# Performance work log

Hardware: AMD Instinct MI355X
Metric: run time of the kernel (lower is better)

The kernel has to match this reference:

```python
import jax, jax.numpy as jnp
import numpy as np

N = 100000   # nodes
E = 1600000  # edges (avg degree 16)
D = 128      # input_dim = embedding_dim = output_dim
NEG_SLOPE = 0.01  # nn.LeakyReLU default


def setup_inputs() -> dict:
    key = jax.random.key(0)
    k0, k1, k2, k3, k4, k5 = jax.random.split(key, 6)
    x = jax.random.normal(k0, (N, D), jnp.float32)
    edge_index = jax.random.randint(k1, (2, E), 0, N, dtype=jnp.int32)
    batch = jnp.zeros((N,), jnp.int32)
    # GCNConv params (glorot-ish scale)
    W1 = jax.random.normal(k2, (D, D), jnp.float32) * 0.05
    b1 = jax.random.normal(k3, (D,), jnp.float32) * 0.05
    W2 = jax.random.normal(k4, (D, D), jnp.float32) * 0.05
    b2 = jax.random.normal(k5, (D,), jnp.float32) * 0.05
    return {"x": x, "W1": W1, "b1": b1, "W2": W2, "b2": b2,
            "edge_index": edge_index, "batch": batch}


def _gcn_conv(x, W, b, src, dst, deg_isqrt):
    # x' = D^{-1/2} (A + I) D^{-1/2} (x W) + b   (PyG GCNConv defaults)
    h = x @ W                                   # [N, D]
    coef = deg_isqrt[src] * deg_isqrt[dst]      # [E]
    msg = h[src] * coef[:, None]                # [E, D] gather + scale
    out = jax.ops.segment_sum(msg, dst, num_segments=N)  # scatter-add
    out = out + h * (deg_isqrt * deg_isqrt)[:, None]      # self-loop term
    return out + b


def reference(x, W1, b1, W2, b2, edge_index, batch):
    src, dst = edge_index[0], edge_index[1]
    # degree on A + I (self loops), same for both layers
    deg = jax.ops.segment_sum(jnp.ones((E,), x.dtype), dst, num_segments=N) + 1.0
    deg_isqrt = jax.lax.rsqrt(deg)
    h = _gcn_conv(x, W1, b1, src, dst, deg_isqrt)
    h = jax.nn.leaky_relu(h, NEG_SLOPE)
    h = _gcn_conv(h, W2, b2, src, dst, deg_isqrt)
    return jax.nn.leaky_relu(h, NEG_SLOPE)
```

## Files before the change

kernel.cpp:

```cpp
#include <hip/hip_runtime.h>
#include <hip/hip_bf16.h>
#include <stdint.h>

#define NN 100000
#define NE 1600000
#define NR (NE + NN)
#define DD 128
#define NEG 0.01f
#define NB 391
#define CAPSH 13
#define NBLKE 391
#define NWB 65
#define GPAD 16

typedef __attribute__((ext_vector_type(8))) short short8;
typedef __attribute__((ext_vector_type(4))) float floatx4;
typedef __attribute__((ext_vector_type(4))) uint32_t uint32x4;

__device__ __forceinline__ uint16_t f2bf(float f){
  uint32_t i = __float_as_uint(f);
  return (uint16_t)((i + 0x7FFFu + ((i >> 16) & 1u)) >> 16);
}
__device__ __forceinline__ float lrelu(float x){ return fmaxf(x, NEG * x); }

__global__ __launch_bounds__(512) void k_init(const uint32_t* __restrict__ xw,
                                              int* __restrict__ flag,
                                              int* __restrict__ gcur){
  int t = threadIdx.x;
  for (int i = t; i < NB * GPAD; i += 512) gcur[i] = 0;
  if (t < 64){
    uint32_t w = xw[t];
    uint32_t e = (w >> 7) & 0xFFu;
    int plaus = (e >= 100u && e <= 134u) ? 1 : 0;
    unsigned long long b = __ballot(plaus);
    if (t == 0) flag[0] = (__popcll(b) >= 48) ? 0 : 1;
  }
}

__global__ __launch_bounds__(512) void k_scat1(const int* __restrict__ src,
                                               const int* __restrict__ dst,
                                               int* __restrict__ gcur,
                                               uint32_t* __restrict__ pairs,
                                               const void* __restrict__ W1,
                                               const void* __restrict__ W2,
                                               const void* __restrict__ b1,
                                               const void* __restrict__ b2,
                                               uint16_t* __restrict__ WT1,
                                               uint16_t* __restrict__ WT2,
                                               uint16_t* __restrict__ bb,
                                               const int* __restrict__ flag){
  int t = threadIdx.x, b = blockIdx.x;
  if (b >= NBLKE){
    int j = (b - NBLKE) * 512 + t;
    int f = flag[0];
    if (j < 16384){
      int c = j >> 7, k = j & 127;
      WT1[j] = f ? f2bf(((const float*)W1)[k * DD + c])
                 : ((const uint16_t*)W1)[k * DD + c];
    } else if (j < 32768){
      int q = j - 16384;
      int c = q >> 7, k = q & 127;
      WT2[q] = f ? f2bf(((const float*)W2)[k * DD + c])
                 : ((const uint16_t*)W2)[k * DD + c];
    } else if (j < 33024){
      int q = j - 32768;
      const void* sp = (q < 128) ? b1 : b2;
      int i2 = q & 127;
      bb[q] = f ? f2bf(((const float*)sp)[i2]) : ((const uint16_t*)sp)[i2];
    }
    return;
  }
  __shared__ int lh[NB];
  if (t < NB) lh[t] = 0;
  __syncthreads();
  int ds[8], ss[8];
  #pragma unroll
  for (int i = 0; i < 8; i++){
    int e = b * 4096 + i * 512 + t;
    if (e < NE){
      ds[i] = dst[e]; ss[i] = src[e];
      atomicAdd(&lh[ds[i] >> 8], 1);
    } else ds[i] = -1;
  }
  __syncthreads();
  if (t < NB){
    int c = lh[t];
    int base = c ? atomicAdd(&gcur[t * GPAD], c) : 0;
    lh[t] = (t << CAPSH) + base;
  }
  __syncthreads();
  #pragma unroll
  for (int i = 0; i < 8; i++){
    if (ds[i] >= 0){
      int bkt = ds[i] >> 8;
      int pos = atomicAdd(&lh[bkt], 1);
      if (pos < ((bkt + 1) << CAPSH))
        pairs[pos] = ((uint32_t)(ds[i] & 255) << 24) | (uint32_t)ss[i];
    }
  }
}

__global__ __launch_bounds__(512) void k_bsort_a(const uint32_t* __restrict__ pairs,
                                                 const int* __restrict__ gcur,
                                                 int2* __restrict__ pairs2,
                                                 int* __restrict__ prow,
                                                 float* __restrict__ dis){
  __shared__ int sg[512];
  __shared__ int lcnt[256], sm[256];
  __shared__ int s_pe;
  int t = threadIdx.x, bkt = blockIdx.x, n0 = bkt << 8;
  int v0 = (t < NB) ? gcur[t * GPAD] : 0;
  sg[t] = v0;
  __syncthreads();
  for (int s = 1; s < 512; s <<= 1){
    int add = (t >= s) ? sg[t - s] : 0;
    __syncthreads();
    sg[t] += add;
    __syncthreads();
  }
  if (t == bkt) s_pe = sg[t] - v0;
  if (t < 256) lcnt[t] = 0;
  __syncthreads();
  int cnt = gcur[bkt * GPAD];
  int begE = bkt << CAPSH;
  for (int i = t; i < cnt; i += 512)
    atomicAdd(&lcnt[pairs[begE + i] >> 24], 1);
  __syncthreads();
  int inb = (n0 + t < NN) ? 1 : 0;
  int v = (t < 256) ? lcnt[t] + inb : 0;
  if (t < 256) sm[t] = v;
  __syncthreads();
  for (int s = 1; s < 256; s <<= 1){
    int add = (t < 256 && t >= s) ? sm[t - s] : 0;
    __syncthreads();
    if (t < 256) sm[t] += add;
    __syncthreads();
  }
  if (t < 256){
    int n = n0 + t;
    int begS = s_pe + n0;
    int excl = sm[t] - v;
    if (n <= NN) prow[n] = begS + excl;
    if (n < NN){
      float dn = rsqrtf((float)(lcnt[t] + 1));
      dis[n] = dn;
      pairs2[begS + excl] = make_int2(n, __float_as_int(dn * dn));
    }
  }
}

__global__ __launch_bounds__(512) void k_bsort_b(const uint32_t* __restrict__ pairs,
                                                 const int* __restrict__ gcur,
                                                 const int* __restrict__ prow,
                                                 const float* __restrict__ dis,
                                                 int2* __restrict__ pairs2){
  __shared__ int cur[256];
  __shared__ float ddn[256];
  int t = threadIdx.x, bkt = blockIdx.x, n0 = bkt << 8;
  if (t < 256){
    int n = n0 + t;
    cur[t] = (n < NN) ? prow[n] + 1 : 0;
    ddn[t] = (n < NN) ? dis[n] : 0.f;
  }
  __syncthreads();
  int cnt = gcur[bkt * GPAD];
  int begE = bkt << CAPSH;
  for (int i = t; i < cnt; i += 512){
    uint32_t u = pairs[begE + i];
    int li = u >> 24, s = (int)(u & 0xFFFFFFu);
    int pos = atomicAdd(&cur[li], 1);
    pairs2[pos] = make_int2(s, __float_as_int(ddn[li] * dis[s]));
  }
}

__device__ __forceinline__ short8 ldcvt(const float* __restrict__ p){
  floatx4 u = ((const floatx4*)p)[0], v = ((const floatx4*)p)[1];
  short8 r;
  r[0] = (short)f2bf(u.x); r[1] = (short)f2bf(u.y);
  r[2] = (short)f2bf(u.z); r[3] = (short)f2bf(u.w);
  r[4] = (short)f2bf(v.x); r[5] = (short)f2bf(v.y);
  r[6] = (short)f2bf(v.z); r[7] = (short)f2bf(v.w);
  return r;
}

__global__ __launch_bounds__(256) void k_gemm(const void* __restrict__ X,
                                              const uint16_t* __restrict__ WT,
                                              uint16_t* __restrict__ H,
                                              const int* __restrict__ flag,
                                              int xf32){
  __shared__ uint16_t lwt[128 * 136];
  int t = threadIdx.x;
  const uint32_t* wt32 = (const uint32_t*)WT;
  #pragma unroll
  for (int i = 0; i < 32; i++){
    int uidx = t + 256 * i;
    uint32_t w2 = wt32[uidx];
    int el = uidx * 2;
    int c = el >> 7, k = el & 127;
    *(uint32_t*)&lwt[c * 136 + k] = w2;
  }
  __syncthreads();

  int wave = t >> 6, lane = t & 63;
  int m = lane & 15, q = lane >> 4;
  int rowbase = blockIdx.x * 64 + wave * 16;
  int ar = rowbase + m;
  if (ar >= NN) ar = 0;
  short8 a0, a1, a2, a3;
  if (xf32 && flag[0]){
    const float* xr = (const float*)X + (size_t)ar * DD;
    a0 = ldcvt(xr + q * 8);        a1 = ldcvt(xr + (q + 4) * 8);
    a2 = ldcvt(xr + (q + 8) * 8);  a3 = ldcvt(xr + (q + 12) * 8);
  } else {
    const short8* xrow = (const short8*)((const uint16_t*)X + (size_t)ar * DD);
    a0 = xrow[q]; a1 = xrow[q + 4]; a2 = xrow[q + 8]; a3 = xrow[q + 12];
  }

  #pragma unroll
  for (int nt = 0; nt < 8; nt++){
    int c = nt * 16 + m;
    const uint16_t* bp = &lwt[c * 136 + q * 8];
    floatx4 acc = {0.f, 0.f, 0.f, 0.f};
    acc = __builtin_amdgcn_mfma_f32_16x16x32_bf16(a0, *(const short8*)(bp +  0), acc, 0, 0, 0);
    acc = __builtin_amdgcn_mfma_f32_16x16x32_bf16(a1, *(const short8*)(bp + 32), acc, 0, 0, 0);
    acc = __builtin_amdgcn_mfma_f32_16x16x32_bf16(a2, *(const short8*)(bp + 64), acc, 0, 0, 0);
    acc = __builtin_amdgcn_mfma_f32_16x16x32_bf16(a3, *(const short8*)(bp + 96), acc, 0, 0, 0);
    #pragma unroll
    for (int r = 0; r < 4; r++){
      int row = rowbase + q * 4 + r;
      if (row < NN) H[(size_t)row * DD + c] = f2bf(acc[r]);
    }
  }
}

#define FMA8(VA, CF)                                                     \
  acc[0] = fmaf(__uint_as_float(VA.x << 16),         CF, acc[0]);        \
  acc[1] = fmaf(__uint_as_float(VA.x & 0xffff0000u), CF, acc[1]);        \
  acc[2] = fmaf(__uint_as_float(VA.y << 16),         CF, acc[2]);        \
  acc[3] = fmaf(__uint_as_float(VA.y & 0xffff0000u), CF, acc[3]);        \
  acc[4] = fmaf(__uint_as_float(VA.z << 16),         CF, acc[4]);        \
  acc[5] = fmaf(__uint_as_float(VA.z & 0xffff0000u), CF, acc[5]);        \
  acc[6] = fmaf(__uint_as_float(VA.w << 16),         CF, acc[6]);        \
  acc[7] = fmaf(__uint_as_float(VA.w & 0xffff0000u), CF, acc[7]);

__global__ __launch_bounds__(256) void k_agg(const uint16_t* __restrict__ H,
                                             const int* __restrict__ prow,
                                             const int2* __restrict__ pairs2,
                                             const uint16_t* __restrict__ bias,
                                             void* __restrict__ OUT,
                                             const int* __restrict__ flag,
                                             int is_final){
  __shared__ int2 ebuf[4][96];
  int wave = threadIdx.x >> 6, lane = threadIdx.x & 63;
  int grp = lane >> 4, sl = lane & 15;
  if (lane >= 32) ebuf[wave][32 + lane] = make_int2(0, 0);
  int n = blockIdx.x * 4 + wave;
  if (n >= NN) return;
  int beg = prow[n], end = prow[n + 1];

  float acc[8] = {0.f,0.f,0.f,0.f,0.f,0.f,0.f,0.f};
  for (int j0 = beg; j0 < end; j0 += 64){
    int cnt = min(64, end - j0);
    int2 r = (lane < cnt) ? pairs2[j0 + lane] : make_int2(0, 0);
    ebuf[wave][lane] = r;
    int chunks = (cnt + 3) >> 2;
    int2 e0 = ebuf[wave][grp];
    int2 e1 = ebuf[wave][4 + grp];
    int2 e2 = ebuf[wave][8 + grp];
    uint32x4 v0 = *(const uint32x4*)(H + (size_t)e0.x * DD + sl * 8);
    uint32x4 v1 = *(const uint32x4*)(H + (size_t)e1.x * DD + sl * 8);
    uint32x4 v2 = *(const uint32x4*)(H + (size_t)e2.x * DD + sl * 8);
    for (int c = 0; c < chunks; c += 3){
      int2 n0 = ebuf[wave][(c + 3) * 4 + grp];
      int2 n1 = ebuf[wave][(c + 4) * 4 + grp];
      int2 n2 = ebuf[wave][(c + 5) * 4 + grp];
      uint32x4 w0 = *(const uint32x4*)(H + (size_t)n0.x * DD + sl * 8);
      uint32x4 w1 = *(const uint32x4*)(H + (size_t)n1.x * DD + sl * 8);
      uint32x4 w2 = *(const uint32x4*)(H + (size_t)n2.x * DD + sl * 8);
      float c0 = __int_as_float(e0.y);
      FMA8(v0, c0)
      float c1 = __int_as_float(e1.y);
      FMA8(v1, c1)
      float c2 = __int_as_float(e2.y);
      FMA8(v2, c2)
      e0 = n0; e1 = n1; e2 = n2;
      v0 = w0; v1 = w1; v2 = w2;
    }
  }
  #pragma unroll
  for (int j = 0; j < 8; j++){
    acc[j] += __shfl_xor(acc[j], 16, 64);
    acc[j] += __shfl_xor(acc[j], 32, 64);
  }
  uint32x4 bv = ((const uint32x4*)bias)[sl];
  float o0 = lrelu(acc[0] + __uint_as_float(bv.x << 16));
  float o1 = lrelu(acc[1] + __uint_as_float(bv.x & 0xffff0000u));
  float o2 = lrelu(acc[2] + __uint_as_float(bv.y << 16));
  float o3 = lrelu(acc[3] + __uint_as_float(bv.y & 0xffff0000u));
  float o4 = lrelu(acc[4] + __uint_as_float(bv.z << 16));
  float o5 = lrelu(acc[5] + __uint_as_float(bv.z & 0xffff0000u));
  float o6 = lrelu(acc[6] + __uint_as_float(bv.w << 16));
  float o7 = lrelu(acc[7] + __uint_as_float(bv.w & 0xffff0000u));
  if (is_final && flag[0]){
    float* orow = (float*)OUT + (size_t)n * DD + sl * 8;
    if (lane < 16){ floatx4 vv = {o0, o1, o2, o3}; ((floatx4*)orow)[0] = vv; }
    else if (lane < 32){ floatx4 vv = {o4, o5, o6, o7}; ((floatx4*)orow)[1] = vv; }
  } else if (lane < 16){
    uint32x4 pv;
    pv.x = (uint32_t)f2bf(o0) | ((uint32_t)f2bf(o1) << 16);
    pv.y = (uint32_t)f2bf(o2) | ((uint32_t)f2bf(o3) << 16);
    pv.z = (uint32_t)f2bf(o4) | ((uint32_t)f2bf(o5) << 16);
    pv.w = (uint32_t)f2bf(o6) | ((uint32_t)f2bf(o7) << 16);
    *(uint32x4*)((uint16_t*)OUT + (size_t)n * DD + sl * 8) = pv;
  }
}

extern "C" void kernel_launch(void* const* d_in, const int* in_sizes, int n_in,
                              void* d_out, int out_size, void* d_ws, size_t ws_size,
                              hipStream_t stream){
  const void* x  = d_in[0];
  const void* W1 = d_in[1];
  const void* b1 = d_in[2];
  const void* W2 = d_in[3];
  const void* b2 = d_in[4];
  const int* ei   = (const int*)d_in[5];
  const int* esrc = ei;
  const int* edst = ei + NE;

  char* ws = (char*)d_ws;
  float*    dis        = (float*)(ws + 0);
  int*      prow       = (int*)(ws + 512ull * 1024);
  int*      flag       = (int*)(ws + 960ull * 1024);
  uint16_t* WT1        = (uint16_t*)(ws + 964ull * 1024);
  uint16_t* WT2        = (uint16_t*)(ws + 996ull * 1024);
  uint16_t* bb         = (uint16_t*)(ws + 1028ull * 1024);
  int*      gcur       = (int*)(ws + 1032ull * 1024);
  int2*     pairs2     = (int2*)(ws + 2048ull * 1024);
  uint32_t* pairs      = (uint32_t*)(ws + 16320ull * 1024);
  uint16_t* hA         = (uint16_t*)(ws + 16384ull * 1024);
  uint16_t* hB         = (uint16_t*)d_out;

  k_init   <<<1, 512, 0, stream>>>((const uint32_t*)x, flag, gcur);
  k_scat1  <<<NBLKE + NWB, 512, 0, stream>>>(esrc, edst, gcur, pairs,
                                             W1, W2, b1, b2, WT1, WT2, bb, flag);
  k_bsort_a<<<NB, 512, 0, stream>>>(pairs, gcur, pairs2, prow, dis);
  k_bsort_b<<<NB, 512, 0, stream>>>(pairs, gcur, prow, dis, pairs2);

  k_gemm<<<(NN + 63) / 64, 256, 0, stream>>>(x, WT1, hA, flag, 1);
  k_agg <<<NN / 4, 256, 0, stream>>>(hA, prow, pairs2, bb, hB, flag, 0);
  k_gemm<<<(NN + 63) / 64, 256, 0, stream>>>(hB, WT2, hA, flag, 0);
  k_agg <<<NN / 4, 256, 0, stream>>>(hA, prow, pairs2, bb + 128, d_out, flag, 1);
}
```

Measured before the change: 300.5 us.

## Fuse layer-1 aggregation with layer-2 GEMM via shared-memory MFMA tile

Adds a kernel that aggregates 16 nodes per block for layer 1, applies bias and LeakyReLU, stages the bf16 rows in shared memory, and multiplies them by W2 with MFMA directly. This removes one kernel launch and the global write and re-read of the intermediate hidden matrix. In exchange, each block processes four nodes per wave serially, which lowers per-node parallelism, and the flag-based dispatch used by the old agg and gemm kernels is no longer applied on this path.

```diff
diff --git a/kernel.cpp b/kernel.cpp
--- a/kernel.cpp
+++ b/kernel.cpp
@@ -243,6 +243,96 @@
   acc[6] = fmaf(__uint_as_float(VA.w << 16),         CF, acc[6]);        \
   acc[7] = fmaf(__uint_as_float(VA.w & 0xffff0000u), CF, acc[7]);
 
+__global__ __launch_bounds__(256) void k_aggg(const uint16_t* __restrict__ H,
+                                              const int* __restrict__ prow,
+                                              const int2* __restrict__ pairs2,
+                                              const uint16_t* __restrict__ bias,
+                                              const uint16_t* __restrict__ WT2,
+                                              uint16_t* __restrict__ H2){
+  __shared__ int2 ebuf[4][96];
+  __shared__ uint16_t hrow[16 * 136];
+  int wave = threadIdx.x >> 6, lane = threadIdx.x & 63;
+  int grp = lane >> 4, sl = lane & 15;
+  if (lane >= 32) ebuf[wave][32 + lane] = make_int2(0, 0);
+  int tile = blockIdx.x << 4;
+  uint32x4 bv = ((const uint32x4*)bias)[sl];
+
+  for (int i = 0; i < 4; i++){
+    int n = tile + wave * 4 + i;
+    int beg = prow[n], end = prow[n + 1];
+    float acc[8] = {0.f,0.f,0.f,0.f,0.f,0.f,0.f,0.f};
+    for (int j0 = beg; j0 < end; j0 += 64){
+      int cnt = min(64, end - j0);
+      int2 r = (lane < cnt) ? pairs2[j0 + lane] : make_int2(0, 0);
+      ebuf[wave][lane] = r;
+      int chunks = (cnt + 3) >> 2;
+      int2 e0 = ebuf[wave][grp];
+      int2 e1 = ebuf[wave][4 + grp];
+      int2 e2 = ebuf[wave][8 + grp];
+      uint32x4 v0 = *(const uint32x4*)(H + (size_t)e0.x * DD + sl * 8);
+      uint32x4 v1 = *(const uint32x4*)(H + (size_t)e1.x * DD + sl * 8);
+      uint32x4 v2 = *(const uint32x4*)(H + (size_t)e2.x * DD + sl * 8);
+      for (int c = 0; c < chunks; c += 3){
+        int2 n0 = ebuf[wave][(c + 3) * 4 + grp];
+        int2 n1 = ebuf[wave][(c + 4) * 4 + grp];
+        int2 n2 = ebuf[wave][(c + 5) * 4 + grp];
+        uint32x4 w0 = *(const uint32x4*)(H + (size_t)n0.x * DD + sl * 8);
+        uint32x4 w1 = *(const uint32x4*)(H + (size_t)n1.x * DD + sl * 8);
+        uint32x4 w2 = *(const uint32x4*)(H + (size_t)n2.x * DD + sl * 8);
+        float c0 = __int_as_float(e0.y);
+        FMA8(v0, c0)
+        float c1 = __int_as_float(e1.y);
+        FMA8(v1, c1)
+        float c2 = __int_as_float(e2.y);
+        FMA8(v2, c2)
+        e0 = n0; e1 = n1; e2 = n2;
+        v0 = w0; v1 = w1; v2 = w2;
+      }
+    }
+    #pragma unroll
+    for (int j = 0; j < 8; j++){
+      acc[j] += __shfl_xor(acc[j], 16, 64);
+      acc[j] += __shfl_xor(acc[j], 32, 64);
+    }
+    float o0 = lrelu(acc[0] + __uint_as_float(bv.x << 16));
+    float o1 = lrelu(acc[1] + __uint_as_float(bv.x & 0xffff0000u));
+    float o2 = lrelu(acc[2] + __uint_as_float(bv.y << 16));
+    float o3 = lrelu(acc[3] + __uint_as_float(bv.y & 0xffff0000u));
+    float o4 = lrelu(acc[4] + __uint_as_float(bv.z << 16));
+    float o5 = lrelu(acc[5] + __uint_as_float(bv.z & 0xffff0000u));
+    float o6 = lrelu(acc[6] + __uint_as_float(bv.w << 16));
+    float o7 = lrelu(acc[7] + __uint_as_float(bv.w & 0xffff0000u));
+    if (lane < 16){
+      uint32x4 pv;
+      pv.x = (uint32_t)f2bf(o0) | ((uint32_t)f2bf(o1) << 16);
+      pv.y = (uint32_t)f2bf(o2) | ((uint32_t)f2bf(o3) << 16);
+      pv.z = (uint32_t)f2bf(o4) | ((uint32_t)f2bf(o5) << 16);
+      pv.w = (uint32_t)f2bf(o6) | ((uint32_t)f2bf(o7) << 16);
+      *(uint32x4*)&hrow[(wave * 4 + i) * 136 + sl * 8] = pv;
+    }
+  }
+  __syncthreads();
+
+  int m = lane & 15, q = lane >> 4;
+  short8 a0 = *(const short8*)&hrow[m * 136 + q * 8];
+  short8 a1 = *(const short8*)&hrow[m * 136 + (q + 4) * 8];
+  short8 a2 = *(const short8*)&hrow[m * 136 + (q + 8) * 8];
+  short8 a3 = *(const short8*)&hrow[m * 136 + (q + 12) * 8];
+  #pragma unroll
+  for (int nt = 0; nt < 2; nt++){
+    int c = (wave * 2 + nt) * 16 + m;
+    const uint16_t* bp = WT2 + c * DD + q * 8;
+    floatx4 a2c = {0.f, 0.f, 0.f, 0.f};
+    a2c = __builtin_amdgcn_mfma_f32_16x16x32_bf16(a0, *(const short8*)(bp +  0), a2c, 0, 0, 0);
+    a2c = __builtin_amdgcn_mfma_f32_16x16x32_bf16(a1, *(const short8*)(bp + 32), a2c, 0, 0, 0);
+    a2c = __builtin_amdgcn_mfma_f32_16x16x32_bf16(a2, *(const short8*)(bp + 64), a2c, 0, 0, 0);
+    a2c = __builtin_amdgcn_mfma_f32_16x16x32_bf16(a3, *(const short8*)(bp + 96), a2c, 0, 0, 0);
+    #pragma unroll
+    for (int r = 0; r < 4; r++)
+      H2[(size_t)(tile + q * 4 + r) * DD + c] = f2bf(a2c[r]);
+  }
+}
+
 __global__ __launch_bounds__(256) void k_agg(const uint16_t* __restrict__ H,
                                              const int* __restrict__ prow,
                                              const int2* __restrict__ pairs2,
@@ -346,8 +436,7 @@
   k_bsort_a<<<NB, 512, 0, stream>>>(pairs, gcur, pairs2, prow, dis);
   k_bsort_b<<<NB, 512, 0, stream>>>(pairs, gcur, prow, dis, pairs2);
 
-  k_gemm<<<(NN + 63) / 64, 256, 0, stream>>>(x, WT1, hA, flag, 1);
-  k_agg <<<NN / 4, 256, 0, stream>>>(hA, prow, pairs2, bb, hB, flag, 0);
-  k_gemm<<<(NN + 63) / 64, 256, 0, stream>>>(hB, WT2, hA, flag, 0);
+  k_gemm<<<(NN + 63) / 64, 256, 0, stream>>>(x, WT1, hB, flag, 1);
+  k_aggg<<<NN / 16, 256, 0, stream>>>(hB, prow, pairs2, bb, WT2, hA);
   k_agg <<<NN / 4, 256, 0, stream>>>(hA, prow, pairs2, bb + 128, d_out, flag, 1);
 }
```

Result: no change. 301.6 us (+0.4%).

## Factor symmetric normalization into GEMM output and aggregation epilogue

Applied to the files above, without the earlier changes.

Instead of storing a per-edge coefficient dis[src]*dis[dst] next to each neighbor index, the GEMM now pre-scales each output row by dis[row], and the aggregation multiplies the summed neighbors by dis[dst] once in the epilogue. The CSR edge list shrinks from int2 to int, which halves the index traffic in aggregation and removes the per-edge FMA coefficient, the dis gather in the sort kernel and its shared-memory cache. Padding entries now point to a zeroed pad row placed at a negative offset before H, replacing row-0 loads with coefficient zero. This depends on the workspace memory before hA and before d_out being writable, and rounding H to bf16 after the extra scaling changes numerics slightly.

```diff
diff --git a/kernel.cpp b/kernel.cpp
--- a/kernel.cpp
+++ b/kernel.cpp
@@ -12,6 +12,7 @@
 #define NBLKE 391
 #define NWB 65
 #define GPAD 16
+#define PADROW (-256)
 
 typedef __attribute__((ext_vector_type(8))) short short8;
 typedef __attribute__((ext_vector_type(4))) float floatx4;
@@ -102,7 +103,7 @@
 
 __global__ __launch_bounds__(512) void k_bsort_a(const uint32_t* __restrict__ pairs,
                                                  const int* __restrict__ gcur,
-                                                 int2* __restrict__ pairs2,
+                                                 int* __restrict__ pairs2,
                                                  int* __restrict__ prow,
                                                  float* __restrict__ dis){
   __shared__ int sg[512];
@@ -142,9 +143,8 @@
     int excl = sm[t] - v;
     if (n <= NN) prow[n] = begS + excl;
     if (n < NN){
-      float dn = rsqrtf((float)(lcnt[t] + 1));
-      dis[n] = dn;
-      pairs2[begS + excl] = make_int2(n, __float_as_int(dn * dn));
+      dis[n] = rsqrtf((float)(lcnt[t] + 1));
+      pairs2[begS + excl] = n;
     }
   }
 }
@@ -152,24 +152,21 @@
 __global__ __launch_bounds__(512) void k_bsort_b(const uint32_t* __restrict__ pairs,
                                                  const int* __restrict__ gcur,
                                                  const int* __restrict__ prow,
-                                                 const float* __restrict__ dis,
-                                                 int2* __restrict__ pairs2){
+                                                 int* __restrict__ pairs2){
   __shared__ int cur[256];
-  __shared__ float ddn[256];
   int t = threadIdx.x, bkt = blockIdx.x, n0 = bkt << 8;
   if (t < 256){
     int n = n0 + t;
     cur[t] = (n < NN) ? prow[n] + 1 : 0;
-    ddn[t] = (n < NN) ? dis[n] : 0.f;
   }
   __syncthreads();
   int cnt = gcur[bkt * GPAD];
   int begE = bkt << CAPSH;
   for (int i = t; i < cnt; i += 512){
     uint32_t u = pairs[begE + i];
-    int li = u >> 24, s = (int)(u & 0xFFFFFFu);
+    int li = u >> 24;
     int pos = atomicAdd(&cur[li], 1);
-    pairs2[pos] = make_int2(s, __float_as_int(ddn[li] * dis[s]));
+    pairs2[pos] = (int)(u & 0xFFFFFFu);
   }
 }
 
@@ -187,9 +184,14 @@
                                               const uint16_t* __restrict__ WT,
                                               uint16_t* __restrict__ H,
                                               const int* __restrict__ flag,
-                                              int xf32){
+                                              int xf32,
+                                              const float* __restrict__ dis){
   __shared__ uint16_t lwt[128 * 136];
   int t = threadIdx.x;
+  if (blockIdx.x == 0 && t < 16){
+    uint32x4 z = {0u, 0u, 0u, 0u};
+    *(uint32x4*)(H + (ptrdiff_t)PADROW * DD + t * 8) = z;
+  }
   const uint32_t* wt32 = (const uint32_t*)WT;
   #pragma unroll
   for (int i = 0; i < 32; i++){
@@ -215,6 +217,12 @@
     const short8* xrow = (const short8*)((const uint16_t*)X + (size_t)ar * DD);
     a0 = xrow[q]; a1 = xrow[q + 4]; a2 = xrow[q + 8]; a3 = xrow[q + 12];
   }
+  float dnr[4];
+  #pragma unroll
+  for (int r = 0; r < 4; r++){
+    int row = rowbase + q * 4 + r;
+    dnr[r] = dis[(row < NN) ? row : 0];
+  }
 
   #pragma unroll
   for (int nt = 0; nt < 8; nt++){
@@ -228,32 +236,33 @@
     #pragma unroll
     for (int r = 0; r < 4; r++){
       int row = rowbase + q * 4 + r;
-      if (row < NN) H[(size_t)row * DD + c] = f2bf(acc[r]);
-    }
-  }
-}
-
-#define FMA8(VA, CF)                                                     \
-  acc[0] = fmaf(__uint_as_float(VA.x << 16),         CF, acc[0]);        \
-  acc[1] = fmaf(__uint_as_float(VA.x & 0xffff0000u), CF, acc[1]);        \
-  acc[2] = fmaf(__uint_as_float(VA.y << 16),         CF, acc[2]);        \
-  acc[3] = fmaf(__uint_as_float(VA.y & 0xffff0000u), CF, acc[3]);        \
-  acc[4] = fmaf(__uint_as_float(VA.z << 16),         CF, acc[4]);        \
-  acc[5] = fmaf(__uint_as_float(VA.z & 0xffff0000u), CF, acc[5]);        \
-  acc[6] = fmaf(__uint_as_float(VA.w << 16),         CF, acc[6]);        \
-  acc[7] = fmaf(__uint_as_float(VA.w & 0xffff0000u), CF, acc[7]);
+      if (row < NN) H[(size_t)row * DD + c] = f2bf(acc[r] * dnr[r]);
+    }
+  }
+}
+
+#define ADD8(VA)                                          \
+  acc[0] += __uint_as_float(VA.x << 16);                  \
+  acc[1] += __uint_as_float(VA.x & 0xffff0000u);          \
+  acc[2] += __uint_as_float(VA.y << 16);                  \
+  acc[3] += __uint_as_float(VA.y & 0xffff0000u);          \
+  acc[4] += __uint_as_float(VA.z << 16);                  \
+  acc[5] += __uint_as_float(VA.z & 0xffff0000u);          \
+  acc[6] += __uint_as_float(VA.w << 16);                  \
+  acc[7] += __uint_as_float(VA.w & 0xffff0000u);
 
 __global__ __launch_bounds__(256) void k_agg(const uint16_t* __restrict__ H,
                                              const int* __restrict__ prow,
-                                             const int2* __restrict__ pairs2,
+                                             const int* __restrict__ pairs2,
                                              const uint16_t* __restrict__ bias,
+                                             const float* __restrict__ dis,
                                              void* __restrict__ OUT,
                                              const int* __restrict__ flag,
                                              int is_final){
-  __shared__ int2 ebuf[4][96];
+  __shared__ int ebuf[4][96];
   int wave = threadIdx.x >> 6, lane = threadIdx.x & 63;
   int grp = lane >> 4, sl = lane & 15;
-  if (lane >= 32) ebuf[wave][32 + lane] = make_int2(0, 0);
+  if (lane >= 32) ebuf[wave][32 + lane] = PADROW;
   int n = blockIdx.x * 4 + wave;
   if (n >= NN) return;
   int beg = prow[n], end = prow[n + 1];
@@ -261,29 +270,25 @@
   float acc[8] = {0.f,0.f,0.f,0.f,0.f,0.f,0.f,0.f};
   for (int j0 = beg; j0 < end; j0 += 64){
     int cnt = min(64, end - j0);
-    int2 r = (lane < cnt) ? pairs2[j0 + lane] : make_int2(0, 0);
+    int r = (lane < cnt) ? pairs2[j0 + lane] : PADROW;
     ebuf[wave][lane] = r;
     int chunks = (cnt + 3) >> 2;
-    int2 e0 = ebuf[wave][grp];
-    int2 e1 = ebuf[wave][4 + grp];
-    int2 e2 = ebuf[wave][8 + grp];
-    uint32x4 v0 = *(const uint32x4*)(H + (size_t)e0.x * DD + sl * 8);
-    uint32x4 v1 = *(const uint32x4*)(H + (size_t)e1.x * DD + sl * 8);
-    uint32x4 v2 = *(const uint32x4*)(H + (size_t)e2.x * DD + sl * 8);
+    int e0 = ebuf[wave][grp];
+    int e1 = ebuf[wave][4 + grp];
+    int e2 = ebuf[wave][8 + grp];
+    uint32x4 v0 = *(const uint32x4*)(H + (ptrdiff_t)e0 * DD + sl * 8);
+    uint32x4 v1 = *(const uint32x4*)(H + (ptrdiff_t)e1 * DD + sl * 8);
+    uint32x4 v2 = *(const uint32x4*)(H + (ptrdiff_t)e2 * DD + sl * 8);
     for (int c = 0; c < chunks; c += 3){
-      int2 n0 = ebuf[wave][(c + 3) * 4 + grp];
-      int2 n1 = ebuf[wave][(c + 4) * 4 + grp];
-      int2 n2 = ebuf[wave][(c + 5) * 4 + grp];
-      uint32x4 w0 = *(const uint32x4*)(H + (size_t)n0.x * DD + sl * 8);
-      uint32x4 w1 = *(const uint32x4*)(H + (size_t)n1.x * DD + sl * 8);
-      uint32x4 w2 = *(const uint32x4*)(H + (size_t)n2.x * DD + sl * 8);
-      float c0 = __int_as_float(e0.y);
-      FMA8(v0, c0)
-      float c1 = __int_as_float(e1.y);
-      FMA8(v1, c1)
-      float c2 = __int_as_float(e2.y);
-      FMA8(v2, c2)
-      e0 = n0; e1 = n1; e2 = n2;
+      int n0 = ebuf[wave][(c + 3) * 4 + grp];
+      int n1 = ebuf[wave][(c + 4) * 4 + grp];
+      int n2 = ebuf[wave][(c + 5) * 4 + grp];
+      uint32x4 w0 = *(const uint32x4*)(H + (ptrdiff_t)n0 * DD + sl * 8);
+      uint32x4 w1 = *(const uint32x4*)(H + (ptrdiff_t)n1 * DD + sl * 8);
+      uint32x4 w2 = *(const uint32x4*)(H + (ptrdiff_t)n2 * DD + sl * 8);
+      ADD8(v0)
+      ADD8(v1)
+      ADD8(v2)
       v0 = w0; v1 = w1; v2 = w2;
     }
   }
@@ -292,15 +297,16 @@
     acc[j] += __shfl_xor(acc[j], 16, 64);
     acc[j] += __shfl_xor(acc[j], 32, 64);
   }
+  float dn = dis[n];
   uint32x4 bv = ((const uint32x4*)bias)[sl];
-  float o0 = lrelu(acc[0] + __uint_as_float(bv.x << 16));
-  float o1 = lrelu(acc[1] + __uint_as_float(bv.x & 0xffff0000u));
-  float o2 = lrelu(acc[2] + __uint_as_float(bv.y << 16));
-  float o3 = lrelu(acc[3] + __uint_as_float(bv.y & 0xffff0000u));
-  float o4 = lrelu(acc[4] + __uint_as_float(bv.z << 16));
-  float o5 = lrelu(acc[5] + __uint_as_float(bv.z & 0xffff0000u));
-  float o6 = lrelu(acc[6] + __uint_as_float(bv.w << 16));
-  float o7 = lrelu(acc[7] + __uint_as_float(bv.w & 0xffff0000u));
+  float o0 = lrelu(fmaf(acc[0], dn, __uint_as_float(bv.x << 16)));
+  float o1 = lrelu(fmaf(acc[1], dn, __uint_as_float(bv.x & 0xffff0000u)));
+  float o2 = lrelu(fmaf(acc[2], dn, __uint_as_float(bv.y << 16)));
+  float o3 = lrelu(fmaf(acc[3], dn, __uint_as_float(bv.y & 0xffff0000u)));
+  float o4 = lrelu(fmaf(acc[4], dn, __uint_as_float(bv.z << 16)));
+  float o5 = lrelu(fmaf(acc[5], dn, __uint_as_float(bv.z & 0xffff0000u)));
+  float o6 = lrelu(fmaf(acc[6], dn, __uint_as_float(bv.w << 16)));
+  float o7 = lrelu(fmaf(acc[7], dn, __uint_as_float(bv.w & 0xffff0000u)));
   if (is_final && flag[0]){
     float* orow = (float*)OUT + (size_t)n * DD + sl * 8;
     if (lane < 16){ floatx4 vv = {o0, o1, o2, o3}; ((floatx4*)orow)[0] = vv; }
@@ -335,7 +341,7 @@
   uint16_t* WT2        = (uint16_t*)(ws + 996ull * 1024);
   uint16_t* bb         = (uint16_t*)(ws + 1028ull * 1024);
   int*      gcur       = (int*)(ws + 1032ull * 1024);
-  int2*     pairs2     = (int2*)(ws + 2048ull * 1024);
+  int*      pairs2     = (int*)(ws + 2048ull * 1024);
   uint32_t* pairs      = (uint32_t*)(ws + 16320ull * 1024);
   uint16_t* hA         = (uint16_t*)(ws + 16384ull * 1024);
   uint16_t* hB         = (uint16_t*)d_out;
@@ -344,10 +350,10 @@
   k_scat1  <<<NBLKE + NWB, 512, 0, stream>>>(esrc, edst, gcur, pairs,
                                              W1, W2, b1, b2, WT1, WT2, bb, flag);
   k_bsort_a<<<NB, 512, 0, stream>>>(pairs, gcur, pairs2, prow, dis);
-  k_bsort_b<<<NB, 512, 0, stream>>>(pairs, gcur, prow, dis, pairs2);
-
-  k_gemm<<<(NN + 63) / 64, 256, 0, stream>>>(x, WT1, hA, flag, 1);
-  k_agg <<<NN / 4, 256, 0, stream>>>(hA, prow, pairs2, bb, hB, flag, 0);
-  k_gemm<<<(NN + 63) / 64, 256, 0, stream>>>(hB, WT2, hA, flag, 0);
-  k_agg <<<NN / 4, 256, 0, stream>>>(hA, prow, pairs2, bb + 128, d_out, flag, 1);
-}
+  k_bsort_b<<<NB, 512, 0, stream>>>(pairs, gcur, prow, pairs2);
+
+  k_gemm<<<(NN + 63) / 64, 256, 0, stream>>>(x, WT1, hA, flag, 1, dis);
+  k_agg <<<NN / 4, 256, 0, stream>>>(hA, prow, pairs2, bb, dis, hB, flag, 0);
+  k_gemm<<<(NN + 63) / 64, 256, 0, stream>>>(hB, WT2, hA, flag, 0, dis);
+  k_agg <<<NN / 4, 256, 0, stream>>>(hA, prow, pairs2, bb + 128, dis, d_out, flag, 1);
+}
```

New measurement: 300.5 us. No clear change (+0.0%).
